# Performance work log

Measured on AMD Instinct MI355X. Metric: run time of the kernel, lower is better.

Reference implementation:

```python
import jax, jax.numpy as jnp
import numpy as np

N_NODES = 50000
N_EDGES = 1600000
NODE_DIM = 64
EDGE_DIM = 64
HID = 64
EPS = 1e-5


def _linear(x, W, b):
    return x @ W + b


def _layernorm(x, g, b):
    m = jnp.mean(x, axis=-1, keepdims=True)
    v = jnp.mean((x - m) ** 2, axis=-1, keepdims=True)
    return (x - m) * jax.lax.rsqrt(v + EPS) * g + b


def _mlp(x, p, pre):
    # Linear-ReLU, Linear-ReLU, Linear-LayerNorm
    h = jax.nn.relu(_linear(x, p[pre + 'W1'], p[pre + 'b1']))
    h = jax.nn.relu(_linear(h, p[pre + 'W2'], p[pre + 'b2']))
    h = _linear(h, p[pre + 'W3'], p[pre + 'b3'])
    return _layernorm(h, p[pre + 'g'], p[pre + 'beta'])


def setup_inputs() -> dict:
    key = jax.random.key(0)
    ks = jax.random.split(key, 16)
    inp = {
        'node_feat': jax.random.normal(ks[0], (N_NODES, NODE_DIM), jnp.float32),
        'edge_feat': jax.random.normal(ks[1], (N_EDGES, EDGE_DIM), jnp.float32),
        'edge_idx': jax.random.randint(ks[2], (N_EDGES, 2), 0, N_NODES, jnp.int32),
        'node_size': N_NODES,
    }
    s = 0.05
    e_in = EDGE_DIM + 2 * NODE_DIM
    n_in = NODE_DIM + EDGE_DIM
    inp['eW1'] = jax.random.normal(ks[3], (e_in, HID), jnp.float32) * s
    inp['eb1'] = jnp.zeros((HID,), jnp.float32)
    inp['eW2'] = jax.random.normal(ks[4], (HID, HID), jnp.float32) * s
    inp['eb2'] = jnp.zeros((HID,), jnp.float32)
    inp['eW3'] = jax.random.normal(ks[5], (HID, HID), jnp.float32) * s
    inp['eb3'] = jnp.zeros((HID,), jnp.float32)
    inp['eg'] = jnp.ones((HID,), jnp.float32)
    inp['ebeta'] = jnp.zeros((HID,), jnp.float32)
    inp['nW1'] = jax.random.normal(ks[6], (n_in, HID), jnp.float32) * s
    inp['nb1'] = jnp.zeros((HID,), jnp.float32)
    inp['nW2'] = jax.random.normal(ks[7], (HID, HID), jnp.float32) * s
    inp['nb2'] = jnp.zeros((HID,), jnp.float32)
    inp['nW3'] = jax.random.normal(ks[8], (HID, HID), jnp.float32) * s
    inp['nb3'] = jnp.zeros((HID,), jnp.float32)
    inp['ng'] = jnp.ones((HID,), jnp.float32)
    inp['nbeta'] = jnp.zeros((HID,), jnp.float32)
    return inp


def reference(node_feat, edge_feat, edge_idx, node_size,
              eW1, eb1, eW2, eb2, eW3, eb3, eg, ebeta,
              nW1, nb1, nW2, nb2, nW3, nb3, ng, nbeta):
    p = dict(eW1=eW1, eb1=eb1, eW2=eW2, eb2=eb2, eW3=eW3, eb3=eb3, eg=eg, ebeta=ebeta,
             nW1=nW1, nb1=nb1, nW2=nW2, nb2=nb2, nW3=nW3, nb3=nb3, ng=ng, nbeta=nbeta)
    center = edge_idx[:, 0]
    source = edge_idx[:, 1]
    # [E, edge_dim + 2*node_dim]
    stacked = jnp.concatenate([edge_feat, node_feat[center], node_feat[source]], axis=1)
    proc_edge_feat = _mlp(stacked, p, 'e')  # [E, 64]
    # scatter-add aggregate to nodes
    nodal_edge_feat = jax.ops.segment_sum(proc_edge_feat, center, num_segments=node_size)
    stacked_node = jnp.concatenate([node_feat, nodal_edge_feat], axis=1)  # [N, node_dim+64]
    proc_node_feat = _mlp(stacked_node, p, 'n')  # [N, 64]
    return proc_edge_feat, proc_node_feat
```

## Files before the change

### kernel.cpp

```cpp
#include <hip/hip_runtime.h>

typedef unsigned short u16;
typedef unsigned int u32;
typedef __attribute__((ext_vector_type(8))) __bf16 bf16x8;
typedef __attribute__((ext_vector_type(4))) float f32x4;
typedef __attribute__((ext_vector_type(2))) u32 u32x2;
typedef __attribute__((ext_vector_type(4))) u32 u32x4;

__device__ __forceinline__ u16 f2bf(float f) {
    u32 u = __float_as_uint(f);
    u = (u + 0x7FFFu + ((u >> 16) & 1u)) >> 16;
    return (u16)u;
}
__device__ __forceinline__ bf16x8 cvt2bf(f32x4 lo, f32x4 hi) {
    bf16x8 r;
    r[0] = (__bf16)lo[0]; r[1] = (__bf16)lo[1]; r[2] = (__bf16)lo[2]; r[3] = (__bf16)lo[3];
    r[4] = (__bf16)hi[0]; r[5] = (__bf16)hi[1]; r[6] = (__bf16)hi[2]; r[7] = (__bf16)hi[3];
    return r;
}
__device__ __forceinline__ bf16x8 load8f_bf(const float* p) {
    return cvt2bf(*(const f32x4*)p, *(const f32x4*)(p + 4));
}
__device__ __forceinline__ u32 pk2(float x, float y) {
    __bf16 bx = (__bf16)x, by = (__bf16)y;
    return (u32)__builtin_bit_cast(u16, bx) | ((u32)__builtin_bit_cast(u16, by) << 16);
}

#define PK_EW1 0
#define PK_EW2 12288
#define PK_EW3 16384
#define PK_NW1 20480
#define PK_NW2 28672
#define PK_NW3 32768
#define PK_TOTAL 36864
#define EW_U16 20480

__global__ void pack_weights_kernel(const float* __restrict__ eW1, const float* __restrict__ eW2,
                                    const float* __restrict__ eW3, const float* __restrict__ nW1,
                                    const float* __restrict__ nW2, const float* __restrict__ nW3,
                                    u16* __restrict__ P) {
    int idx = blockIdx.x * blockDim.x + threadIdx.x;
    if (idx >= PK_TOTAL) return;
    const float* W; int base;
    if (idx < PK_EW2)      { W = eW1; base = PK_EW1; }
    else if (idx < PK_EW3) { W = eW2; base = PK_EW2; }
    else if (idx < PK_NW1) { W = eW3; base = PK_EW3; }
    else if (idx < PK_NW2) { W = nW1; base = PK_NW1; }
    else if (idx < PK_NW3) { W = nW2; base = PK_NW2; }
    else                   { W = nW3; base = PK_NW3; }
    int r = idx - base;
    int j = r & 7, lane = (r >> 3) & 63, m = (r >> 9) & 3, s = r >> 11;
    int k = s * 32 + (lane >> 4) * 8 + j;
    int col = 16 * m + (lane & 15);
    P[idx] = f2bf(W[k * 64 + col]);
}

__global__ void degree_kernel(const int* __restrict__ edge_idx, int* __restrict__ deg, int E) {
    int e = blockIdx.x * blockDim.x + threadIdx.x;
    if (e < E) atomicAdd(&deg[edge_idx[2 * e]], 1);
}

__global__ void scan_blocks_kernel(const int* __restrict__ deg, int* __restrict__ off,
                                   int* __restrict__ partials, int N) {
    __shared__ int sh[256];
    const int t = threadIdx.x;
    const int g = blockIdx.x * 256 + t;
    int v = (g < N) ? deg[g] : 0;
    sh[t] = v;
    __syncthreads();
#pragma unroll
    for (int d = 1; d < 256; d <<= 1) {
        int add = (t >= d) ? sh[t - d] : 0;
        __syncthreads();
        sh[t] += add;
        __syncthreads();
    }
    if (g < N) off[g] = sh[t] - v;
    if (t == 255) partials[blockIdx.x] = sh[255];
}

__global__ void scan_partials_kernel(int* __restrict__ partials, int nparts) {
    __shared__ int sh[256];
    const int t = threadIdx.x;
    int v = (t < nparts) ? partials[t] : 0;
    sh[t] = v;
    __syncthreads();
#pragma unroll
    for (int d = 1; d < 256; d <<= 1) {
        int add = (t >= d) ? sh[t - d] : 0;
        __syncthreads();
        sh[t] += add;
        __syncthreads();
    }
    if (t < nparts) partials[t] = sh[t] - v;
}

__global__ void finalize_offsets_kernel(int* __restrict__ off, int* __restrict__ pos,
                                        const int* __restrict__ partials, int N, int E) {
    int g = blockIdx.x * blockDim.x + threadIdx.x;
    if (g < N) {
        int o = off[g] + partials[g >> 8];
        off[g] = o;
        pos[g] = o;
    }
    if (g == 0) off[N] = E;
}

__global__ void fill_csr_kernel(const int* __restrict__ edge_idx, int* __restrict__ pos,
                                int* __restrict__ csr, int E) {
    int e = blockIdx.x * blockDim.x + threadIdx.x;
    if (e < E) {
        int slot = atomicAdd(&pos[edge_idx[2 * e]], 1);
        csr[slot] = e;
    }
}

__global__ __launch_bounds__(256) void gather_kernel(
    const float* __restrict__ proc_edge, const int* __restrict__ off,
    const int* __restrict__ csr, u16* __restrict__ nodal16, int N)
{
    const int wid = threadIdx.x >> 6, lane = threadIdx.x & 63;
    const int n = blockIdx.x * 4 + wid;
    if (n >= N) return;
    const int r = lane >> 4;
    const int q = lane & 15;
    const int beg = off[n], end = off[n + 1];
    f32x4 v0 = 0.0f, v1 = 0.0f;
    int j = beg + r;
    for (; j + 4 < end; j += 8) {
        int e0 = csr[j], e1 = csr[j + 4];
        v0 += *(const f32x4*)(proc_edge + (size_t)e0 * 64 + q * 4);
        v1 += *(const f32x4*)(proc_edge + (size_t)e1 * 64 + q * 4);
    }
    if (j < end) {
        int e0 = csr[j];
        v0 += *(const f32x4*)(proc_edge + (size_t)e0 * 64 + q * 4);
    }
    v0 += v1;
#pragma unroll
    for (int i = 0; i < 4; ++i) {
        v0[i] += __shfl_xor(v0[i], 16, 64);
        v0[i] += __shfl_xor(v0[i], 32, 64);
    }
    if (r == 0) {
        u32x2 pv; pv[0] = pk2(v0[0], v0[1]); pv[1] = pk2(v0[2], v0[3]);
        *(u32x2*)(nodal16 + (size_t)n * 64 + q * 4) = pv;
    }
}

#define ET 2
__global__ __launch_bounds__(256) void edge_mlp_kernel(
    const float* __restrict__ node_feat, const float* __restrict__ edge_feat,
    const int* __restrict__ edge_idx, const u16* __restrict__ Pw,
    const float* __restrict__ b1g, const float* __restrict__ b2g, const float* __restrict__ b3g,
    const float* __restrict__ gg, const float* __restrict__ betag,
    float* __restrict__ out_edge, int E)
{
    __shared__ u16 wlds[EW_U16];
    __shared__ u16 htile[4][1024];
    __shared__ float params[5][64];
    const int tid = threadIdx.x;
#pragma unroll
    for (int i = 0; i < 10; ++i) {
        u32x4 v = *(const u32x4*)(Pw + (size_t)(i * 256 + tid) * 8);
        *(u32x4*)(wlds + (size_t)(i * 256 + tid) * 8) = v;
    }
    if (tid < 64) {
        params[0][tid] = b1g[tid];
        params[1][tid] = b2g[tid];
        params[2][tid] = b3g[tid];
        params[3][tid] = gg[tid];
        params[4][tid] = betag[tid];
    }
    __syncthreads();

    const int wid = tid >> 6, lane = tid & 63;
    const int er = lane & 15, a = lane >> 4;
    const int ebase = (blockIdx.x * 4 + wid) * (16 * ET);
    if (ebase >= E) return;
    u16* ht = htile[wid];
    const int swz = (er & 7) << 4;

    int eidx[ET], cn[ET], sn[ET];
#pragma unroll
    for (int t = 0; t < ET; ++t) {
        int e = ebase + t * 16 + er;
        if (e > E - 1) e = E - 1;
        eidx[t] = e;
        int2 ii = *(const int2*)(edge_idx + 2 * e);
        cn[t] = ii.x; sn[t] = ii.y;
    }

    f32x4 acc[ET][4];
#pragma unroll
    for (int t = 0; t < ET; ++t)
#pragma unroll
        for (int m = 0; m < 4; ++m) acc[t][m] = 0.0f;

#pragma unroll
    for (int t = 0; t < ET; ++t) {
        f32x4 raw[12];
#pragma unroll
        for (int s = 0; s < 6; ++s) {
            const float* src;
            if (s < 2)      src = edge_feat + (size_t)eidx[t] * 64 + s * 32 + a * 8;
            else if (s < 4) src = node_feat + (size_t)cn[t] * 64 + (s - 2) * 32 + a * 8;
            else            src = node_feat + (size_t)sn[t] * 64 + (s - 4) * 32 + a * 8;
            raw[2 * s]     = *(const f32x4*)src;
            raw[2 * s + 1] = *(const f32x4*)(src + 4);
        }
#pragma unroll
        for (int s = 0; s < 6; ++s) {
            bf16x8 bf = cvt2bf(raw[2 * s], raw[2 * s + 1]);
#pragma unroll
            for (int m = 0; m < 4; ++m) {
                bf16x8 af = *(const bf16x8*)(wlds + PK_EW1 + ((s * 4 + m) * 64 + lane) * 8);
                acc[t][m] = __builtin_amdgcn_mfma_f32_16x16x32_bf16(af, bf, acc[t][m], 0, 0, 0);
            }
        }
    }

#pragma unroll
    for (int t = 0; t < ET; ++t) {
#pragma unroll
        for (int m = 0; m < 4; ++m) {
            float v0 = fmaxf(acc[t][m][0] + params[0][16 * m + 4 * a + 0], 0.0f);
            float v1 = fmaxf(acc[t][m][1] + params[0][16 * m + 4 * a + 1], 0.0f);
            float v2 = fmaxf(acc[t][m][2] + params[0][16 * m + 4 * a + 2], 0.0f);
            float v3 = fmaxf(acc[t][m][3] + params[0][16 * m + 4 * a + 3], 0.0f);
            u32x2 pv; pv[0] = pk2(v0, v1); pv[1] = pk2(v2, v3);
            int boff = (er * 128 + (16 * m + 4 * a) * 2) ^ swz;
            *(u32x2*)((char*)ht + boff) = pv;
        }
        f32x4 a2[4];
#pragma unroll
        for (int m = 0; m < 4; ++m) a2[m] = 0.0f;
#pragma unroll
        for (int s = 0; s < 2; ++s) {
            int boff = (er * 128 + s * 64 + a * 16) ^ swz;
            bf16x8 bf = *(const bf16x8*)((char*)ht + boff);
#pragma unroll
            for (int m = 0; m < 4; ++m) {
                bf16x8 af = *(const bf16x8*)(wlds + PK_EW2 + ((s * 4 + m) * 64 + lane) * 8);
                a2[m] = __builtin_amdgcn_mfma_f32_16x16x32_bf16(af, bf, a2[m], 0, 0, 0);
            }
        }
#pragma unroll
        for (int m = 0; m < 4; ++m) {
            float v0 = fmaxf(a2[m][0] + params[1][16 * m + 4 * a + 0], 0.0f);
            float v1 = fmaxf(a2[m][1] + params[1][16 * m + 4 * a + 1], 0.0f);
            float v2 = fmaxf(a2[m][2] + params[1][16 * m + 4 * a + 2], 0.0f);
            float v3 = fmaxf(a2[m][3] + params[1][16 * m + 4 * a + 3], 0.0f);
            u32x2 pv; pv[0] = pk2(v0, v1); pv[1] = pk2(v2, v3);
            int boff = (er * 128 + (16 * m + 4 * a) * 2) ^ swz;
            *(u32x2*)((char*)ht + boff) = pv;
        }
        f32x4 a3[4];
#pragma unroll
        for (int m = 0; m < 4; ++m) a3[m] = 0.0f;
#pragma unroll
        for (int s = 0; s < 2; ++s) {
            int boff = (er * 128 + s * 64 + a * 16) ^ swz;
            bf16x8 bf = *(const bf16x8*)((char*)ht + boff);
#pragma unroll
            for (int m = 0; m < 4; ++m) {
                bf16x8 af = *(const bf16x8*)(wlds + PK_EW3 + ((s * 4 + m) * 64 + lane) * 8);
                a3[m] = __builtin_amdgcn_mfma_f32_16x16x32_bf16(af, bf, a3[m], 0, 0, 0);
            }
        }
        float vals[16], sum = 0.0f, ssq = 0.0f;
#pragma unroll
        for (int m = 0; m < 4; ++m)
#pragma unroll
            for (int r = 0; r < 4; ++r) {
                float v = a3[m][r] + params[2][16 * m + 4 * a + r];
                vals[4 * m + r] = v; sum += v; ssq += v * v;
            }
        sum += __shfl_xor(sum, 16, 64); sum += __shfl_xor(sum, 32, 64);
        ssq += __shfl_xor(ssq, 16, 64); ssq += __shfl_xor(ssq, 32, 64);
        const float mean = sum * 0.015625f;
        const float var = ssq * 0.015625f - mean * mean;
        const float inv = rsqrtf(var + 1e-5f);
        const int e = ebase + t * 16 + er;
        if (e < E) {
#pragma unroll
            for (int m = 0; m < 4; ++m) {
                f32x4 o;
#pragma unroll
                for (int r = 0; r < 4; ++r) {
                    int f = 16 * m + 4 * a + r;
                    o[r] = (vals[4 * m + r] - mean) * inv * params[3][f] + params[4][f];
                }
                *(f32x4*)(out_edge + (size_t)e * 64 + 16 * m + 4 * a) = o;
            }
        }
    }
}

__global__ __launch_bounds__(256) void node_mlp_kernel(
    const float* __restrict__ node_feat, const u16* __restrict__ nodal16,
    const u16* __restrict__ Pw,
    const float* __restrict__ b1g, const float* __restrict__ b2g, const float* __restrict__ b3g,
    const float* __restrict__ gg, const float* __restrict__ betag,
    float* __restrict__ out_node, int N)
{
    __shared__ float params[5][64];
    __shared__ u16 htile[4][1024];
    const int tid = threadIdx.x;
    if (tid < 64) {
        params[0][tid] = b1g[tid];
        params[1][tid] = b2g[tid];
        params[2][tid] = b3g[tid];
        params[3][tid] = gg[tid];
        params[4][tid] = betag[tid];
    }
    __syncthreads();
    const int wid = tid >> 6, lane = tid & 63;
    const int er = lane & 15, a = lane >> 4;
    const int nbase = (blockIdx.x * 4 + wid) * 16;
    if (nbase >= N) return;
    const int n = nbase + er;
    u16* ht = htile[wid];
    const int swz = (er & 7) << 4;

    f32x4 acc[4];
#pragma unroll
    for (int m = 0; m < 4; ++m) acc[m] = 0.0f;

#pragma unroll
    for (int s = 0; s < 4; ++s) {
        bf16x8 af[4];
#pragma unroll
        for (int m = 0; m < 4; ++m)
            af[m] = *(const bf16x8*)(Pw + PK_NW1 + ((s * 4 + m) * 64 + lane) * 8);
        bf16x8 bf;
        if (s < 2) bf = load8f_bf(node_feat + (size_t)n * 64 + s * 32 + a * 8);
        else       bf = *(const bf16x8*)(nodal16 + (size_t)n * 64 + (s - 2) * 32 + a * 8);
#pragma unroll
        for (int m = 0; m < 4; ++m)
            acc[m] = __builtin_amdgcn_mfma_f32_16x16x32_bf16(af[m], bf, acc[m], 0, 0, 0);
    }
#pragma unroll
    for (int m = 0; m < 4; ++m) {
        float v0 = fmaxf(acc[m][0] + params[0][16 * m + 4 * a + 0], 0.0f);
        float v1 = fmaxf(acc[m][1] + params[0][16 * m + 4 * a + 1], 0.0f);
        float v2 = fmaxf(acc[m][2] + params[0][16 * m + 4 * a + 2], 0.0f);
        float v3 = fmaxf(acc[m][3] + params[0][16 * m + 4 * a + 3], 0.0f);
        u32x2 pv; pv[0] = pk2(v0, v1); pv[1] = pk2(v2, v3);
        int boff = (er * 128 + (16 * m + 4 * a) * 2) ^ swz;
        *(u32x2*)((char*)ht + boff) = pv;
    }

#pragma unroll
    for (int m = 0; m < 4; ++m) acc[m] = 0.0f;
#pragma unroll
    for (int s = 0; s < 2; ++s) {
        bf16x8 af[4];
#pragma unroll
        for (int m = 0; m < 4; ++m)
            af[m] = *(const bf16x8*)(Pw + PK_NW2 + ((s * 4 + m) * 64 + lane) * 8);
        int boff = (er * 128 + s * 64 + a * 16) ^ swz;
        bf16x8 bf = *(const bf16x8*)((char*)ht + boff);
#pragma unroll
        for (int m = 0; m < 4; ++m)
            acc[m] = __builtin_amdgcn_mfma_f32_16x16x32_bf16(af[m], bf, acc[m], 0, 0, 0);
    }
#pragma unroll
    for (int m = 0; m < 4; ++m) {
        float v0 = fmaxf(acc[m][0] + params[1][16 * m + 4 * a + 0], 0.0f);
        float v1 = fmaxf(acc[m][1] + params[1][16 * m + 4 * a + 1], 0.0f);
        float v2 = fmaxf(acc[m][2] + params[1][16 * m + 4 * a + 2], 0.0f);
        float v3 = fmaxf(acc[m][3] + params[1][16 * m + 4 * a + 3], 0.0f);
        u32x2 pv; pv[0] = pk2(v0, v1); pv[1] = pk2(v2, v3);
        int boff = (er * 128 + (16 * m + 4 * a) * 2) ^ swz;
        *(u32x2*)((char*)ht + boff) = pv;
    }

#pragma unroll
    for (int m = 0; m < 4; ++m) acc[m] = 0.0f;
#pragma unroll
    for (int s = 0; s < 2; ++s) {
        bf16x8 af[4];
#pragma unroll
        for (int m = 0; m < 4; ++m)
            af[m] = *(const bf16x8*)(Pw + PK_NW3 + ((s * 4 + m) * 64 + lane) * 8);
        int boff = (er * 128 + s * 64 + a * 16) ^ swz;
        bf16x8 bf = *(const bf16x8*)((char*)ht + boff);
#pragma unroll
        for (int m = 0; m < 4; ++m)
            acc[m] = __builtin_amdgcn_mfma_f32_16x16x32_bf16(af[m], bf, acc[m], 0, 0, 0);
    }
    float vals[16], sum = 0.0f, ssq = 0.0f;
#pragma unroll
    for (int m = 0; m < 4; ++m)
#pragma unroll
        for (int r = 0; r < 4; ++r) {
            float v = acc[m][r] + params[2][16 * m + 4 * a + r];
            vals[4 * m + r] = v; sum += v; ssq += v * v;
        }
    sum += __shfl_xor(sum, 16, 64); sum += __shfl_xor(sum, 32, 64);
    ssq += __shfl_xor(ssq, 16, 64); ssq += __shfl_xor(ssq, 32, 64);
    const float mean = sum * 0.015625f;
    const float var = ssq * 0.015625f - mean * mean;
    const float inv = rsqrtf(var + 1e-5f);
#pragma unroll
    for (int m = 0; m < 4; ++m) {
        f32x4 o;
#pragma unroll
        for (int r = 0; r < 4; ++r) {
            int f = 16 * m + 4 * a + r;
            o[r] = (vals[4 * m + r] - mean) * inv * params[3][f] + params[4][f];
        }
        *(f32x4*)(out_node + (size_t)n * 64 + 16 * m + 4 * a) = o;
    }
}

extern "C" void kernel_launch(void* const* d_in, const int* in_sizes, int n_in,
                              void* d_out, int out_size, void* d_ws, size_t ws_size,
                              hipStream_t stream) {
    const float* node_feat = (const float*)d_in[0];
    const float* edge_feat = (const float*)d_in[1];
    const int* edge_idx  = (const int*)d_in[2];
    const float* eW1 = (const float*)d_in[4];
    const float* eb1 = (const float*)d_in[5];
    const float* eW2 = (const float*)d_in[6];
    const float* eb2 = (const float*)d_in[7];
    const float* eW3 = (const float*)d_in[8];
    const float* eb3 = (const float*)d_in[9];
    const float* eg  = (const float*)d_in[10];
    const float* ebt = (const float*)d_in[11];
    const float* nW1 = (const float*)d_in[12];
    const float* nb1 = (const float*)d_in[13];
    const float* nW2 = (const float*)d_in[14];
    const float* nb2 = (const float*)d_in[15];
    const float* nW3 = (const float*)d_in[16];
    const float* nb3 = (const float*)d_in[17];
    const float* ng  = (const float*)d_in[18];
    const float* nbt = (const float*)d_in[19];

    const int N = in_sizes[0] / 64;
    const int E = in_sizes[1] / 64;
    const int nparts = (N + 255) / 256;

    char* w = (char*)d_ws;
    int* off      = (int*)w;                    w += (size_t)(N + 1) * 4;
    int* pos      = (int*)w;                    w += (size_t)N * 4;
    int* partials = (int*)w;                    w += 256 * 4;
    int* csr      = (int*)w;                    w += (size_t)E * 4;
    u16* Pw       = (u16*)w;                    w += (size_t)PK_TOTAL * 2;
    u16* nodal16  = (u16*)w;

    float* out_edge = (float*)d_out;
    float* out_node = out_edge + (size_t)E * 64;

    pack_weights_kernel<<<(PK_TOTAL + 255) / 256, 256, 0, stream>>>(eW1, eW2, eW3, nW1, nW2, nW3, Pw);

    const int eblocks = (E + (64 * ET) - 1) / (64 * ET);
    edge_mlp_kernel<<<eblocks, 256, 0, stream>>>(node_feat, edge_feat, edge_idx, Pw,
                                                 eb1, eb2, eb3, eg, ebt, out_edge, E);

    hipMemsetAsync(pos, 0, (size_t)N * 4, stream);
    degree_kernel<<<(E + 255) / 256, 256, 0, stream>>>(edge_idx, pos, E);
    scan_blocks_kernel<<<nparts, 256, 0, stream>>>(pos, off, partials, N);
    scan_partials_kernel<<<1, 256, 0, stream>>>(partials, nparts);
    finalize_offsets_kernel<<<(N + 255) / 256, 256, 0, stream>>>(off, pos, partials, N, E);
    fill_csr_kernel<<<(E + 255) / 256, 256, 0, stream>>>(edge_idx, pos, csr, E);

    gather_kernel<<<(N + 3) / 4, 256, 0, stream>>>(out_edge, off, csr, nodal16, N);

    const int nblocks = (N + 63) / 64;
    node_mlp_kernel<<<nblocks, 256, 0, stream>>>(node_feat, nodal16, Pw,
                                                 nb1, nb2, nb3, ng, nbt, out_node, N);
}
```

Before: 580.3 us.

## Shrink edge MLP LDS footprint with 512-thread blocks and staged weights

The edge MLP kernel now runs 512-thread blocks (8 waves) and keeps only the first-layer weights in LDS. After the first layer it synchronises and overwrites that buffer with the second- and third-layer weights, which cuts shared memory per wave so more waves can be resident. The change adds two block-wide barriers and a mid-kernel reload of weights, and removes the early return. The gather kernel is also unrolled to four independent accumulators to keep more loads in flight.

```diff
diff --git a/kernel.cpp b/kernel.cpp
--- a/kernel.cpp
+++ b/kernel.cpp
@@ -33,7 +33,6 @@
 #define PK_NW2 28672
 #define PK_NW3 32768
 #define PK_TOTAL 36864
-#define EW_U16 20480
 
 __global__ void pack_weights_kernel(const float* __restrict__ eW1, const float* __restrict__ eW2,
                                     const float* __restrict__ eW3, const float* __restrict__ nW1,
@@ -125,18 +124,20 @@
     const int r = lane >> 4;
     const int q = lane & 15;
     const int beg = off[n], end = off[n + 1];
-    f32x4 v0 = 0.0f, v1 = 0.0f;
+    f32x4 v0 = 0.0f, v1 = 0.0f, v2 = 0.0f, v3 = 0.0f;
     int j = beg + r;
-    for (; j + 4 < end; j += 8) {
-        int e0 = csr[j], e1 = csr[j + 4];
+    for (; j + 12 < end; j += 16) {
+        int e0 = csr[j], e1 = csr[j + 4], e2 = csr[j + 8], e3 = csr[j + 12];
         v0 += *(const f32x4*)(proc_edge + (size_t)e0 * 64 + q * 4);
         v1 += *(const f32x4*)(proc_edge + (size_t)e1 * 64 + q * 4);
-    }
-    if (j < end) {
+        v2 += *(const f32x4*)(proc_edge + (size_t)e2 * 64 + q * 4);
+        v3 += *(const f32x4*)(proc_edge + (size_t)e3 * 64 + q * 4);
+    }
+    for (; j < end; j += 4) {
         int e0 = csr[j];
         v0 += *(const f32x4*)(proc_edge + (size_t)e0 * 64 + q * 4);
     }
-    v0 += v1;
+    v0 += v1; v2 += v3; v0 += v2;
 #pragma unroll
     for (int i = 0; i < 4; ++i) {
         v0[i] += __shfl_xor(v0[i], 16, 64);
@@ -149,21 +150,21 @@
 }
 
 #define ET 2
-__global__ __launch_bounds__(256) void edge_mlp_kernel(
+__global__ __launch_bounds__(512, 6) void edge_mlp_kernel(
     const float* __restrict__ node_feat, const float* __restrict__ edge_feat,
     const int* __restrict__ edge_idx, const u16* __restrict__ Pw,
     const float* __restrict__ b1g, const float* __restrict__ b2g, const float* __restrict__ b3g,
     const float* __restrict__ gg, const float* __restrict__ betag,
     float* __restrict__ out_edge, int E)
 {
-    __shared__ u16 wlds[EW_U16];
-    __shared__ u16 htile[4][1024];
+    __shared__ u16 wlds[12288];
+    __shared__ u16 htile[8][1024];
     __shared__ float params[5][64];
     const int tid = threadIdx.x;
 #pragma unroll
-    for (int i = 0; i < 10; ++i) {
-        u32x4 v = *(const u32x4*)(Pw + (size_t)(i * 256 + tid) * 8);
-        *(u32x4*)(wlds + (size_t)(i * 256 + tid) * 8) = v;
+    for (int i = 0; i < 3; ++i) {
+        int idx = i * 512 + tid;
+        *(u32x4*)(wlds + (size_t)idx * 8) = *(const u32x4*)(Pw + PK_EW1 + (size_t)idx * 8);
     }
     if (tid < 64) {
         params[0][tid] = b1g[tid];
@@ -176,8 +177,7 @@
 
     const int wid = tid >> 6, lane = tid & 63;
     const int er = lane & 15, a = lane >> 4;
-    const int ebase = (blockIdx.x * 4 + wid) * (16 * ET);
-    if (ebase >= E) return;
+    const int ebase = (blockIdx.x * 8 + wid) * (16 * ET);
     u16* ht = htile[wid];
     const int swz = (er & 7) << 4;
 
@@ -214,11 +214,18 @@
             bf16x8 bf = cvt2bf(raw[2 * s], raw[2 * s + 1]);
 #pragma unroll
             for (int m = 0; m < 4; ++m) {
-                bf16x8 af = *(const bf16x8*)(wlds + PK_EW1 + ((s * 4 + m) * 64 + lane) * 8);
+                bf16x8 af = *(const bf16x8*)(wlds + ((s * 4 + m) * 64 + lane) * 8);
                 acc[t][m] = __builtin_amdgcn_mfma_f32_16x16x32_bf16(af, bf, acc[t][m], 0, 0, 0);
             }
         }
     }
+    __syncthreads();
+#pragma unroll
+    for (int i = 0; i < 2; ++i) {
+        int idx = i * 512 + tid;
+        *(u32x4*)(wlds + (size_t)idx * 8) = *(const u32x4*)(Pw + PK_EW2 + (size_t)idx * 8);
+    }
+    __syncthreads();
 
 #pragma unroll
     for (int t = 0; t < ET; ++t) {
@@ -241,7 +248,7 @@
             bf16x8 bf = *(const bf16x8*)((char*)ht + boff);
 #pragma unroll
             for (int m = 0; m < 4; ++m) {
-                bf16x8 af = *(const bf16x8*)(wlds + PK_EW2 + ((s * 4 + m) * 64 + lane) * 8);
+                bf16x8 af = *(const bf16x8*)(wlds + ((s * 4 + m) * 64 + lane) * 8);
                 a2[m] = __builtin_amdgcn_mfma_f32_16x16x32_bf16(af, bf, a2[m], 0, 0, 0);
             }
         }
@@ -264,7 +271,7 @@
             bf16x8 bf = *(const bf16x8*)((char*)ht + boff);
 #pragma unroll
             for (int m = 0; m < 4; ++m) {
-                bf16x8 af = *(const bf16x8*)(wlds + PK_EW3 + ((s * 4 + m) * 64 + lane) * 8);
+                bf16x8 af = *(const bf16x8*)(wlds + 4096 + ((s * 4 + m) * 64 + lane) * 8);
                 a3[m] = __builtin_amdgcn_mfma_f32_16x16x32_bf16(af, bf, a3[m], 0, 0, 0);
             }
         }
@@ -455,8 +462,8 @@
 
     pack_weights_kernel<<<(PK_TOTAL + 255) / 256, 256, 0, stream>>>(eW1, eW2, eW3, nW1, nW2, nW3, Pw);
 
-    const int eblocks = (E + (64 * ET) - 1) / (64 * ET);
-    edge_mlp_kernel<<<eblocks, 256, 0, stream>>>(node_feat, edge_feat, edge_idx, Pw,
+    const int eblocks = (E + 255) / 256;
+    edge_mlp_kernel<<<eblocks, 512, 0, stream>>>(node_feat, edge_feat, edge_idx, Pw,
                                                  eb1, eb2, eb3, eg, ebt, out_edge, E);
 
     hipMemsetAsync(pos, 0, (size_t)N * 4, stream);
```

After: 570.6 us. Within noise of the previous version (-1.7%).
